# Performance work log

Hardware: AMD Instinct MI355X
Metric: run time of the kernel (lower is better)

## Reference

```python
import jax, jax.numpy as jnp
import numpy as np

B, S, D, U = 32, 4096, 512, 128

def setup_inputs() -> dict:
    key = jax.random.key(0)
    k1, k2, k3, k4, k5 = jax.random.split(key, 5)
    query = jax.random.normal(k1, (B, D), dtype=jnp.float32)
    values = jax.random.normal(k2, (B, S, D), dtype=jnp.float32)
    s = 1.0 / np.sqrt(D)
    W1 = jax.random.normal(k3, (D, U), dtype=jnp.float32) * s
    W2 = jax.random.normal(k4, (D, U), dtype=jnp.float32) * s
    V = jax.random.normal(k5, (U, 1), dtype=jnp.float32) * (1.0 / np.sqrt(U))
    b1 = jnp.zeros((U,), dtype=jnp.float32)
    b2 = jnp.zeros((U,), dtype=jnp.float32)
    bv = jnp.zeros((1,), dtype=jnp.float32)
    return {"query": query, "values": values, "W1": W1, "b1": b1,
            "W2": W2, "b2": b2, "V": V, "bv": bv}

def reference(query, values, W1, b1, W2, b2, V, bv):
    # query: [B, D] -> [B, 1, U]; values: [B, S, D] -> [B, S, U]
    q_proj = (query @ W1 + b1)[:, None, :]                  # [B, 1, U]
    v_proj = jnp.einsum('bsd,du->bsu', values, W2) + b2      # [B, S, U]
    score = jnp.tanh(q_proj + v_proj) @ V + bv               # [B, S, 1]
    attention_weights = jax.nn.softmax(score, axis=1)        # [B, S, 1]
    context_vector = jnp.sum(attention_weights * values, axis=1)  # [B, D]
    return context_vector, attention_weights
```

## Files before the change

kernel.cpp:

```cpp
#include <hip/hip_runtime.h>
#include <hip/hip_bf16.h>
#include <math.h>

#define NB 32
#define NS 4096
#define ND 512
#define NU 128
#define RR 32
#define NCHUNK (NS / RR)
#define ASTR 520

typedef __bf16 bf16x8 __attribute__((ext_vector_type(8)));
typedef unsigned short u16x8 __attribute__((ext_vector_type(8)));
typedef float f32x4 __attribute__((ext_vector_type(4)));
union FragCvt { u16x8 u; bf16x8 b; };

__device__ inline unsigned short f2bf(float x) {
  union { float f; unsigned u; } v; v.f = x;
  return (unsigned short)((v.u + 0x7FFFu + ((v.u >> 16) & 1u)) >> 16);
}
__device__ inline float bf2f(unsigned int bits16) {
  union { unsigned u; float f; } v; v.u = bits16 << 16;
  return v.f;
}
__device__ inline u16x8 pack8(float4 a, float4 b) {
  u16x8 r;
  r[0] = f2bf(a.x); r[1] = f2bf(a.y); r[2] = f2bf(a.z); r[3] = f2bf(a.w);
  r[4] = f2bf(b.x); r[5] = f2bf(b.y); r[6] = f2bf(b.z); r[7] = f2bf(b.w);
  return r;
}
__device__ inline float fast_tanh(float x) {
  float ex = __expf(2.f * x);
  return 1.f - 2.f / (ex + 1.f);
}

__global__ void prep(const float* __restrict__ q, const float* __restrict__ W1,
                     const float* __restrict__ b1, const float* __restrict__ b2,
                     const float* __restrict__ W2,
                     float* __restrict__ qb, unsigned short* __restrict__ w2t) {
  if (blockIdx.x < 16) {
    int idx = blockIdx.x * 256 + threadIdx.x;
    int b = idx >> 7, u = idx & 127;
    float s = b1[u] + b2[u];
    const float* qr = q + b * ND;
    #pragma unroll 8
    for (int d = 0; d < ND; ++d) s += qr[d] * W1[d * NU + u];
    qb[idx] = s;
  } else {
    int idx = (blockIdx.x - 16) * 256 + threadIdx.x;
    int u = idx >> 9, d = idx & 511;
    w2t[idx] = f2bf(W2[d * NU + u]);
  }
}

__global__ __launch_bounds__(256, 4) void fused_attn(
    const float* __restrict__ values,
    const float* __restrict__ qb,
    const unsigned short* __restrict__ w2t,
    const float* __restrict__ V,
    const float* __restrict__ bvp,
    float* __restrict__ wout,
    float* __restrict__ Cpart,
    float* __restrict__ Lacc)
{
  __shared__ unsigned short Alds[RR * ASTR];
  __shared__ float sbuf[4][32];
  __shared__ float wlds[RR];

  const int tid = threadIdx.x;
  const int b = blockIdx.x >> 7;
  const int chunk = blockIdx.x & 127;
  const int s0 = chunk * RR;
  const int wave = tid >> 6, lane = tid & 63;
  const int quad = lane >> 4, lidx = lane & 15;
  const int ng = wave;

  const float* vbase = values + ((size_t)b * NS + s0) * ND;

  #pragma unroll
  for (int i = 0; i < 8; ++i) {
    int p = tid + 256 * i;
    int row = p >> 6;
    int c8 = p & 63;
    const float* ap = vbase + row * ND + c8 * 8;
    float4 v0 = *(const float4*)ap;
    float4 v1 = *(const float4*)(ap + 4);
    *(u16x8*)(&Alds[row * ASTR + c8 * 8]) = pack8(v0, v1);
  }
  __syncthreads();

  f32x4 acc[2][2];
  #pragma unroll
  for (int mt = 0; mt < 2; ++mt)
    #pragma unroll
    for (int nt = 0; nt < 2; ++nt)
      acc[mt][nt] = (f32x4){0.f, 0.f, 0.f, 0.f};

  const unsigned short* b0p = w2t + (ng * 32 + lidx) * ND + quad * 8;
  const unsigned short* b1p = b0p + 16 * ND;
  const unsigned short* a0p = (const unsigned short*)&Alds[lidx * ASTR + quad * 8];
  const unsigned short* a1p = a0p + 16 * ASTR;

  #pragma unroll 4
  for (int kt = 0; kt < 16; ++kt) {
    FragCvt bf0, bf1, af0, af1;
    bf0.u = *(const u16x8*)(b0p + kt * 32);
    bf1.u = *(const u16x8*)(b1p + kt * 32);
    af0.u = *(const u16x8*)(a0p + kt * 32);
    af1.u = *(const u16x8*)(a1p + kt * 32);
    acc[0][0] = __builtin_amdgcn_mfma_f32_16x16x32_bf16(af0.b, bf0.b, acc[0][0], 0, 0, 0);
    acc[0][1] = __builtin_amdgcn_mfma_f32_16x16x32_bf16(af0.b, bf1.b, acc[0][1], 0, 0, 0);
    acc[1][0] = __builtin_amdgcn_mfma_f32_16x16x32_bf16(af1.b, bf0.b, acc[1][0], 0, 0, 0);
    acc[1][1] = __builtin_amdgcn_mfma_f32_16x16x32_bf16(af1.b, bf1.b, acc[1][1], 0, 0, 0);
  }

  float part[2][4] = {{0.f,0.f,0.f,0.f},{0.f,0.f,0.f,0.f}};
  #pragma unroll
  for (int nt = 0; nt < 2; ++nt) {
    const int col = ng * 32 + nt * 16 + lidx;
    const float qv = qb[b * NU + col];
    const float vv = V[col];
    #pragma unroll
    for (int mt = 0; mt < 2; ++mt)
      #pragma unroll
      for (int r = 0; r < 4; ++r)
        part[mt][r] += fast_tanh(acc[mt][nt][r] + qv) * vv;
  }
  #pragma unroll
  for (int m = 1; m <= 8; m <<= 1)
    #pragma unroll
    for (int mt = 0; mt < 2; ++mt)
      #pragma unroll
      for (int r = 0; r < 4; ++r)
        part[mt][r] += __shfl_xor(part[mt][r], m, 64);
  if (lidx == 0) {
    #pragma unroll
    for (int mt = 0; mt < 2; ++mt)
      #pragma unroll
      for (int r = 0; r < 4; ++r)
        sbuf[ng][mt * 16 + quad * 4 + r] = part[mt][r];
  }
  __syncthreads();

  if (tid < 32) {
    float s = sbuf[0][tid] + sbuf[1][tid] + sbuf[2][tid] + sbuf[3][tid];
    float e = expf(s + *bvp);
    wout[(size_t)b * NS + s0 + tid] = e;
    wlds[tid] = e;
    float es = e;
    #pragma unroll
    for (int m = 1; m <= 16; m <<= 1) es += __shfl_xor(es, m, 64);
    if (tid == 0) atomicAdd(Lacc + b, es);
  }
  __syncthreads();

  const int d0 = tid * 2;
  float c0 = 0.f, c1 = 0.f;
  #pragma unroll 8
  for (int r = 0; r < RR; ++r) {
    float w = wlds[r];
    unsigned int pk = *(const unsigned int*)(&Alds[r * ASTR + d0]);
    c0 += w * bf2f(pk & 0xFFFFu);
    c1 += w * bf2f(pk >> 16);
  }
  float* cp = Cpart + (size_t)blockIdx.x * ND + d0;
  cp[0] = c0;
  cp[1] = c1;
}

__global__ void finalize(const float* __restrict__ Cpart, const float* __restrict__ Lacc,
                         float* __restrict__ out) {
  int idx = blockIdx.x * 256 + threadIdx.x;
  if (idx < NB * ND) {
    int b = idx >> 9, d = idx & 511;
    const float* p = Cpart + (size_t)b * NCHUNK * ND + d;
    float a0 = 0.f, a1 = 0.f, a2 = 0.f, a3 = 0.f;
    #pragma unroll 4
    for (int c = 0; c < NCHUNK; c += 4) {
      a0 += p[(size_t)(c + 0) * ND];
      a1 += p[(size_t)(c + 1) * ND];
      a2 += p[(size_t)(c + 2) * ND];
      a3 += p[(size_t)(c + 3) * ND];
    }
    out[idx] = (a0 + a1 + a2 + a3) / Lacc[b];
  } else {
    int j = idx - NB * ND;
    int b = j >> 12;
    out[idx] = out[idx] / Lacc[b];
  }
}

extern "C" void kernel_launch(void* const* d_in, const int* in_sizes, int n_in,
                              void* d_out, int out_size, void* d_ws, size_t ws_size,
                              hipStream_t stream) {
  const float* query  = (const float*)d_in[0];
  const float* values = (const float*)d_in[1];
  const float* W1     = (const float*)d_in[2];
  const float* b1     = (const float*)d_in[3];
  const float* W2     = (const float*)d_in[4];
  const float* b2     = (const float*)d_in[5];
  const float* V      = (const float*)d_in[6];
  const float* bv     = (const float*)d_in[7];
  float* out = (float*)d_out;

  char* ws = (char*)d_ws;
  float* Cpart = (float*)ws;
  float* Lacc  = (float*)(ws + 8388608);
  float* qbuf  = (float*)(ws + 8389120);
  unsigned short* w2t = (unsigned short*)(ws + 8405504);

  hipMemsetAsync(Lacc, 0, 512, stream);

  prep<<<272, 256, 0, stream>>>(query, W1, b1, b2, W2, qbuf, w2t);
  fused_attn<<<NB * NCHUNK, 256, 0, stream>>>(values, qbuf, w2t, V, bv,
                                              out + NB * ND, Cpart, Lacc);
  finalize<<<576, 256, 0, stream>>>(Cpart, Lacc, out);
}
```

Before: 450.1 us.

## Process two chunks per block with register prefetch of the next chunk

Each block now handles two consecutive 32-row chunks and halves the grid. While the MFMA, tanh and softmax work runs on the first chunk, the second chunk's values are prefetched from global memory into registers (64 floats per thread). Once the first chunk is done they are packed into LDS. This is meant to hide global load latency behind compute. It costs higher register pressure, so launch bounds drop to 3 blocks per SIMD, and there is less block-level parallelism.

Result: slower. 463.4 us (+2.9%).

```diff
diff --git a/kernel.cpp b/kernel.cpp
--- a/kernel.cpp
+++ b/kernel.cpp
@@ -53,7 +53,7 @@
   }
 }
 
-__global__ __launch_bounds__(256, 4) void fused_attn(
+__global__ __launch_bounds__(256, 3) void fused_attn(
     const float* __restrict__ values,
     const float* __restrict__ qb,
     const unsigned short* __restrict__ w2t,
@@ -68,20 +68,21 @@
   __shared__ float wlds[RR];
 
   const int tid = threadIdx.x;
-  const int b = blockIdx.x >> 7;
-  const int chunk = blockIdx.x & 127;
-  const int s0 = chunk * RR;
+  const int blk = blockIdx.x;
+  const int b = blk >> 6;
+  const int chunk0 = (blk & 63) * 2;
+  const int s0 = chunk0 * RR;
   const int wave = tid >> 6, lane = tid & 63;
   const int quad = lane >> 4, lidx = lane & 15;
   const int ng = wave;
 
   const float* vbase = values + ((size_t)b * NS + s0) * ND;
 
+  const int srow = tid >> 6;
   #pragma unroll
   for (int i = 0; i < 8; ++i) {
     int p = tid + 256 * i;
-    int row = p >> 6;
-    int c8 = p & 63;
+    int row = p >> 6, c8 = p & 63;
     const float* ap = vbase + row * ND + c8 * 8;
     float4 v0 = *(const float4*)ap;
     float4 v1 = *(const float4*)(ap + 4);
@@ -89,83 +90,112 @@
   }
   __syncthreads();
 
-  f32x4 acc[2][2];
-  #pragma unroll
-  for (int mt = 0; mt < 2; ++mt)
-    #pragma unroll
-    for (int nt = 0; nt < 2; ++nt)
-      acc[mt][nt] = (f32x4){0.f, 0.f, 0.f, 0.f};
-
   const unsigned short* b0p = w2t + (ng * 32 + lidx) * ND + quad * 8;
   const unsigned short* b1p = b0p + 16 * ND;
   const unsigned short* a0p = (const unsigned short*)&Alds[lidx * ASTR + quad * 8];
   const unsigned short* a1p = a0p + 16 * ASTR;
-
-  #pragma unroll 4
-  for (int kt = 0; kt < 16; ++kt) {
-    FragCvt bf0, bf1, af0, af1;
-    bf0.u = *(const u16x8*)(b0p + kt * 32);
-    bf1.u = *(const u16x8*)(b1p + kt * 32);
-    af0.u = *(const u16x8*)(a0p + kt * 32);
-    af1.u = *(const u16x8*)(a1p + kt * 32);
-    acc[0][0] = __builtin_amdgcn_mfma_f32_16x16x32_bf16(af0.b, bf0.b, acc[0][0], 0, 0, 0);
-    acc[0][1] = __builtin_amdgcn_mfma_f32_16x16x32_bf16(af0.b, bf1.b, acc[0][1], 0, 0, 0);
-    acc[1][0] = __builtin_amdgcn_mfma_f32_16x16x32_bf16(af1.b, bf0.b, acc[1][0], 0, 0, 0);
-    acc[1][1] = __builtin_amdgcn_mfma_f32_16x16x32_bf16(af1.b, bf1.b, acc[1][1], 0, 0, 0);
-  }
-
-  float part[2][4] = {{0.f,0.f,0.f,0.f},{0.f,0.f,0.f,0.f}};
-  #pragma unroll
-  for (int nt = 0; nt < 2; ++nt) {
-    const int col = ng * 32 + nt * 16 + lidx;
-    const float qv = qb[b * NU + col];
-    const float vv = V[col];
+  const float qv0 = qb[b * NU + ng * 32 + lidx];
+  const float qv1 = qb[b * NU + ng * 32 + 16 + lidx];
+  const float vv0 = V[ng * 32 + lidx];
+  const float vv1 = V[ng * 32 + 16 + lidx];
+
+  float4 pre[16];
+
+  #pragma unroll 1
+  for (int cc = 0; cc < 2; ++cc) {
+    if (cc == 0) {
+      const float* v1b = vbase + 32 * ND;
+      #pragma unroll
+      for (int i = 0; i < 8; ++i) {
+        int p = tid + 256 * i;
+        int row = p >> 6, c8 = p & 63;
+        const float* ap = v1b + row * ND + c8 * 8;
+        pre[2 * i]     = *(const float4*)ap;
+        pre[2 * i + 1] = *(const float4*)(ap + 4);
+      }
+    }
+
+    f32x4 acc[2][2];
     #pragma unroll
     for (int mt = 0; mt < 2; ++mt)
       #pragma unroll
-      for (int r = 0; r < 4; ++r)
-        part[mt][r] += fast_tanh(acc[mt][nt][r] + qv) * vv;
-  }
-  #pragma unroll
-  for (int m = 1; m <= 8; m <<= 1)
+      for (int nt = 0; nt < 2; ++nt)
+        acc[mt][nt] = (f32x4){0.f, 0.f, 0.f, 0.f};
+
+    #pragma unroll 4
+    for (int kt = 0; kt < 16; ++kt) {
+      FragCvt bf0, bf1, af0, af1;
+      bf0.u = *(const u16x8*)(b0p + kt * 32);
+      bf1.u = *(const u16x8*)(b1p + kt * 32);
+      af0.u = *(const u16x8*)(a0p + kt * 32);
+      af1.u = *(const u16x8*)(a1p + kt * 32);
+      acc[0][0] = __builtin_amdgcn_mfma_f32_16x16x32_bf16(af0.b, bf0.b, acc[0][0], 0, 0, 0);
+      acc[0][1] = __builtin_amdgcn_mfma_f32_16x16x32_bf16(af0.b, bf1.b, acc[0][1], 0, 0, 0);
+      acc[1][0] = __builtin_amdgcn_mfma_f32_16x16x32_bf16(af1.b, bf0.b, acc[1][0], 0, 0, 0);
+      acc[1][1] = __builtin_amdgcn_mfma_f32_16x16x32_bf16(af1.b, bf1.b, acc[1][1], 0, 0, 0);
+    }
+
+    float part[2][4] = {{0.f,0.f,0.f,0.f},{0.f,0.f,0.f,0.f}};
     #pragma unroll
     for (int mt = 0; mt < 2; ++mt)
       #pragma unroll
-      for (int r = 0; r < 4; ++r)
-        part[mt][r] += __shfl_xor(part[mt][r], m, 64);
-  if (lidx == 0) {
+      for (int r = 0; r < 4; ++r) {
+        part[mt][r] += fast_tanh(acc[mt][0][r] + qv0) * vv0;
+        part[mt][r] += fast_tanh(acc[mt][1][r] + qv1) * vv1;
+      }
     #pragma unroll
-    for (int mt = 0; mt < 2; ++mt)
-      #pragma unroll
-      for (int r = 0; r < 4; ++r)
-        sbuf[ng][mt * 16 + quad * 4 + r] = part[mt][r];
-  }
-  __syncthreads();
-
-  if (tid < 32) {
-    float s = sbuf[0][tid] + sbuf[1][tid] + sbuf[2][tid] + sbuf[3][tid];
-    float e = expf(s + *bvp);
-    wout[(size_t)b * NS + s0 + tid] = e;
-    wlds[tid] = e;
-    float es = e;
-    #pragma unroll
-    for (int m = 1; m <= 16; m <<= 1) es += __shfl_xor(es, m, 64);
-    if (tid == 0) atomicAdd(Lacc + b, es);
-  }
-  __syncthreads();
-
-  const int d0 = tid * 2;
-  float c0 = 0.f, c1 = 0.f;
-  #pragma unroll 8
-  for (int r = 0; r < RR; ++r) {
-    float w = wlds[r];
-    unsigned int pk = *(const unsigned int*)(&Alds[r * ASTR + d0]);
-    c0 += w * bf2f(pk & 0xFFFFu);
-    c1 += w * bf2f(pk >> 16);
-  }
-  float* cp = Cpart + (size_t)blockIdx.x * ND + d0;
-  cp[0] = c0;
-  cp[1] = c1;
+    for (int m = 1; m <= 8; m <<= 1)
+      #pragma unroll
+      for (int mt = 0; mt < 2; ++mt)
+        #pragma unroll
+        for (int r = 0; r < 4; ++r)
+          part[mt][r] += __shfl_xor(part[mt][r], m, 64);
+    if (lidx == 0) {
+      #pragma unroll
+      for (int mt = 0; mt < 2; ++mt)
+        #pragma unroll
+        for (int r = 0; r < 4; ++r)
+          sbuf[ng][mt * 16 + quad * 4 + r] = part[mt][r];
+    }
+    __syncthreads();
+
+    if (tid < 32) {
+      float s = sbuf[0][tid] + sbuf[1][tid] + sbuf[2][tid] + sbuf[3][tid];
+      float e = expf(s + *bvp);
+      wout[(size_t)b * NS + (chunk0 + cc) * RR + tid] = e;
+      wlds[tid] = e;
+      float es = e;
+      #pragma unroll
+      for (int m = 1; m <= 16; m <<= 1) es += __shfl_xor(es, m, 64);
+      if (tid == 0) atomicAdd(Lacc + b, es);
+    }
+    __syncthreads();
+
+    const int d0 = tid * 2;
+    float c0 = 0.f, c1 = 0.f;
+    #pragma unroll 8
+    for (int r = 0; r < RR; ++r) {
+      float w = wlds[r];
+      unsigned int pk = *(const unsigned int*)(&Alds[r * ASTR + d0]);
+      c0 += w * bf2f(pk & 0xFFFFu);
+      c1 += w * bf2f(pk >> 16);
+    }
+    float* cp = Cpart + ((size_t)b * NCHUNK + chunk0 + cc) * ND + d0;
+    cp[0] = c0;
+    cp[1] = c1;
+
+    if (cc == 0) {
+      __syncthreads();
+      #pragma unroll
+      for (int i = 0; i < 8; ++i) {
+        int p = tid + 256 * i;
+        int row = p >> 6, c8 = p & 63;
+        *(u16x8*)(&Alds[row * ASTR + c8 * 8]) = pack8(pre[2 * i], pre[2 * i + 1]);
+      }
+      __syncthreads();
+    }
+  }
+  (void)srow;
 }
 
 __global__ void finalize(const float* __restrict__ Cpart, const float* __restrict__ Lacc,
@@ -212,7 +242,7 @@
   hipMemsetAsync(Lacc, 0, 512, stream);
 
   prep<<<272, 256, 0, stream>>>(query, W1, b1, b2, W2, qbuf, w2t);
-  fused_attn<<<NB * NCHUNK, 256, 0, stream>>>(values, qbuf, w2t, V, bv,
-                                              out + NB * ND, Cpart, Lacc);
+  fused_attn<<<NB * 64, 256, 0, stream>>>(values, qbuf, w2t, V, bv,
+                                          out + NB * ND, Cpart, Lacc);
   finalize<<<576, 256, 0, stream>>>(Cpart, Lacc, out);
 }
```
